# Performance work log

Hardware: AMD Instinct MI355X
Metric: run time of the kernel (lower is better)

Reference implementation:

```python
import jax, jax.numpy as jnp
import numpy as np

B, C, H, W = 64, 256, 14, 14
K = 9
HID = 256   # EdgeAgg hidden_channels = in_channels
OUT = 512   # out_channels = 2*in_channels (required by final reshape)


def _knn(q, kset, k):
    # ViG dense_knn_matrix: squared-distance knn, top-k of -dist (self-loop may be included)
    qs = jnp.sum(q * q, -1)
    ks = jnp.sum(kset * kset, -1)
    dist = qs[:, :, None] - 2.0 * jnp.einsum('bnc,bmc->bnm', q, kset) + ks[:, None, :]
    _, idx = jax.lax.top_k(-dist, k)   # (B,N,k) neighbor indices into kset
    return idx


def _edgeconv_add(feat, nbr, validf, w, b):
    # PyG EdgeConv(nn=Linear, aggr='add') with per-node valid-edge mask:
    #   out[i] = sum_{j in valid nbrs(i)} cat(x_i, x_j - x_i) @ w + b
    # nn is linear, so aggregate neighbor diffs BEFORE the matmul (same math, less traffic).
    Cf = feat.shape[-1]
    wa, wb = w[:Cf], w[Cf:]
    deg = jnp.sum(validf, -1, keepdims=True)                   # (B,N,1)
    xj = feat[jnp.arange(feat.shape[0])[:, None, None], nbr]   # (B,N,k,C) gather
    sum_xj = jnp.einsum('bnkc,bnk->bnc', xj, validf)
    return deg * (feat @ wa + b) + (sum_xj - deg * feat) @ wb


def _forward(x, fc1_w, fc1_b, fc2_w, fc2_b, fce_w, fce_b, inout_w, inout_b,
             attn_w, attn_b, upd_w, upd_b, kp_w, kp_b, enc_w, enc_b,
             mu_w, mu_b, dec_w, dec_b, T):
    k = dec_w.shape[-1]
    b_, c_, h_, w_ = x.shape
    n = h_ * w_
    xs = x.reshape(b_, c_, n)                       # (B,C,N)
    x_sp = jnp.transpose(xs, (0, 2, 1))             # (B,N,C) true spatial node feats for knn
    x_sp_d = jax.lax.stop_gradient(x_sp)            # original detaches before knn
    x_nbr = _knn(x_sp_d, x_sp_d, k)
    # temporal roll across the T frames of each clip
    y_sp = jnp.roll(x_sp.reshape(b_ // T, T, n, c_), -1, axis=1).reshape(b_, n, c_)
    y_nbr = _knn(x_sp_d, jax.lax.stop_gradient(y_sp), k)
    # faithful to original: x.view(B*N, C) reinterprets the contiguous (B,C,N) buffer
    x_feat = xs.reshape(b_, n, c_)
    y_feat = jnp.transpose(y_sp, (0, 2, 1)).reshape(b_, n, c_)
    # VAE-like K predictor (deterministic z = mu); argmax -> per-node degree in [0,k)
    hk = x_feat.reshape(b_ * n, c_) @ kp_w + kp_b
    hk = jax.nn.relu(hk @ enc_w + enc_b)
    mu = hk @ mu_w + mu_b
    logits = mu @ dec_w + dec_b                     # (B*N, k)
    k_int = jnp.argmax(logits, axis=1)
    # generate_mask: keep the first k_int[i] of node i's k edges
    validf = (jnp.arange(k)[None, :] < k_int[:, None]).astype(x.dtype).reshape(b_, n, k)

    def edge_agg(feat, nbr):
        h1 = jax.nn.relu(_edgeconv_add(feat, nbr, validf, fc1_w, fc1_b))
        h2 = _edgeconv_add(h1, nbr, validf, fc2_w, fc2_b)
        return (h2 @ fce_w + fce_b).reshape(b_ * n, -1)

    x_agg = edge_agg(x_feat, x_nbr)
    y_agg = edge_agg(y_feat, y_nbr)
    scores = (jnp.concatenate([x_agg, y_agg], -1) @ attn_w + attn_b)[:, 0]
    wgt = jax.nn.softmax(scores, axis=0)[:, None]   # softmax over ALL B*N nodes (as in source)
    fused = wgt * x_agg + (1.0 - wgt) * y_agg
    xin = x_feat.reshape(b_ * n, c_) @ inout_w + inout_b
    upd = jax.nn.relu(jnp.concatenate([xin, fused], -1) @ upd_w + upd_b)   # (B*N, 2C)
    return jnp.transpose(upd.reshape(b_, n, 2 * c_), (0, 2, 1)).reshape(b_, 2 * c_, h_, w_)


def setup_inputs():
    key = jax.random.key(0)
    ks = iter(jax.random.split(key, 32))

    def lin(i, o):
        return jax.random.normal(next(ks), (i, o), jnp.float32) / np.sqrt(i)

    def bias(o):
        return jax.random.normal(next(ks), (o,), jnp.float32) * 0.01

    return {
        'x': jax.random.normal(next(ks), (B, C, H, W), jnp.float32),
        'fc1_w': lin(2 * C, HID), 'fc1_b': bias(HID),
        'fc2_w': lin(2 * HID, HID), 'fc2_b': bias(HID),
        'fce_w': lin(HID, OUT), 'fce_b': bias(OUT),
        'inout_w': lin(C, OUT), 'inout_b': bias(OUT),
        'attn_w': lin(2 * OUT, 1), 'attn_b': bias(1),
        'upd_w': lin(2 * OUT, OUT), 'upd_b': bias(OUT),
        'kp_w': lin(C, 500), 'kp_b': bias(500),
        'enc_w': lin(500, 64), 'enc_b': bias(64),
        'mu_w': lin(64, 32), 'mu_b': bias(32),
        'dec_w': lin(32, K), 'dec_b': bias(K),
        'T': 16,
    }


def reference(x, fc1_w, fc1_b, fc2_w, fc2_b, fce_w, fce_b, inout_w, inout_b,
              attn_w, attn_b, upd_w, upd_b, kp_w, kp_b, enc_w, enc_b,
              mu_w, mu_b, dec_w, dec_b, T):
    return _forward(x, fc1_w, fc1_b, fc2_w, fc2_b, fce_w, fce_b, inout_w, inout_b,
                    attn_w, attn_b, upd_w, upd_b, kp_w, kp_b, enc_w, enc_b,
                    mu_w, mu_b, dec_w, dec_b, T)
```

## Files before the change

### kernel.cpp

```cpp
#include <hip/hip_runtime.h>
#include <cstddef>
#include <cstdint>

constexpr int BATCH = 64;
constexpr int CH    = 256;
constexpr int NPT   = 196;
constexpr int ROWS  = BATCH * NPT;
constexpr int BSTRIDE = CH * NPT;
constexpr int KNB   = 8;
constexpr int DSTR  = 208;

typedef __bf16 bf16x8 __attribute__((ext_vector_type(8)));
typedef __bf16 bf16x4 __attribute__((ext_vector_type(4)));
typedef _Float16 f16x8 __attribute__((ext_vector_type(8)));
typedef float  f32x4  __attribute__((ext_vector_type(4)));
typedef unsigned long long u64;

__device__ __forceinline__ int src_batch(int b) {
    return (b & ~15) | ((b + 1) & 15);
}

__device__ __forceinline__ void gload_lds16(const void* g, void* l) {
    __builtin_amdgcn_global_load_lds(
        (const __attribute__((address_space(1))) void*)g,
        (__attribute__((address_space(3))) void*)l, 16, 0, 0);
}

__device__ __forceinline__ int xcd_swz(int lin, int nwg) {
    int q = nwg >> 3;
    return (lin & 7) * q + (lin >> 3);
}

__global__ __launch_bounds__(256) void front_kernel(const float* __restrict__ x,
        _Float16* __restrict__ XH, _Float16* __restrict__ XL,
        __bf16* __restrict__ XB, float* __restrict__ qsp,
        const float* __restrict__ fc1_w, const float* __restrict__ fc2_w,
        const float* __restrict__ fce_w, const float* __restrict__ upd_w,
        const float* __restrict__ kp_w, const float* __restrict__ kp_b,
        const float* __restrict__ enc_w, const float* __restrict__ enc_b,
        const float* __restrict__ mu_w, const float* __restrict__ mu_b,
        const float* __restrict__ dec_w, const float* __restrict__ dec_b,
        const float* __restrict__ inout_w, const float* __restrict__ inout_b,
        const float* __restrict__ upd_b,
        __bf16* __restrict__ W1catT, __bf16* __restrict__ W2catT,
        __bf16* __restrict__ fcet, __bf16* __restrict__ updC,
        float* __restrict__ KW1, float* __restrict__ kb1,
        float* __restrict__ KW2, float* __restrict__ kb2,
        float* __restrict__ bcomp, int* __restrict__ smcnt) {
    __shared__ __attribute__((aligned(16))) char smem[16896];
    float (*tile)[65] = (float(*)[65])smem;
    int bid = blockIdx.x;
    int t = threadIdx.x;
    if (bid < 1024) {
        int m0 = (bid & 3) * 64, c0 = ((bid >> 2) & 3) * 64, b = bid >> 4;
        const float* xb = x + (size_t)b * BSTRIDE;
        #pragma unroll
        for (int s = 0; s < 16; ++s) {
            int idx = s * 256 + t;
            int cc = idx >> 6, mm = idx & 63;
            int m = m0 + mm;
            float v = (m < NPT) ? xb[(size_t)(c0 + cc) * NPT + m] : 0.f;
            tile[cc][mm] = v;
            if (m < NPT)
                XB[(size_t)b * BSTRIDE + (size_t)(c0 + cc) * NPT + m] = (__bf16)v;
        }
        __syncthreads();
        #pragma unroll
        for (int s = 0; s < 16; ++s) {
            int idx = s * 256 + t;
            int mm = idx >> 6, cc = idx & 63;
            float v = tile[cc][mm];
            _Float16 h = (_Float16)v;
            size_t off = ((size_t)b * 256 + (m0 + mm)) * 256 + c0 + cc;
            XH[off] = h;
            XL[off] = (_Float16)(v - (float)h);
        }
        if (t < 64) {
            float acc = 0.f;
            #pragma unroll
            for (int cc = 0; cc < 64; ++cc) {
                float v = tile[cc][t];
                acc = fmaf(v, v, acc);
            }
            qsp[(size_t)(c0 >> 6) * 16384 + b * 256 + m0 + t] = acc;
        }
    } else {
        int pbid = bid - 1024;
        if (pbid == 0 && t == 0) smcnt[0] = 0;
        if (pbid < 64) {
            const float* W = (pbid < 32) ? fc1_w : fc2_w;
            __bf16* WT = (pbid < 32) ? W1catT : W2catT;
            int local = pbid & 31;
            int n0 = (local >> 2) * 64, k0 = (local & 3) * 64;
            #pragma unroll
            for (int s = 0; s < 16; ++s) {
                int idx = s * 256 + t;
                int kk = idx >> 6, nn = idx & 63;
                float v;
                if (n0 < 256)
                    v = W[(size_t)(k0 + kk) * 256 + n0 + nn] -
                        W[(size_t)(k0 + kk + 256) * 256 + n0 + nn];
                else
                    v = W[(size_t)(k0 + kk + 256) * 256 + (n0 - 256) + nn];
                tile[kk][nn] = v;
            }
            __syncthreads();
            #pragma unroll
            for (int s = 0; s < 16; ++s) {
                int idx = s * 256 + t;
                int nn = idx >> 6, kk = idx & 63;
                WT[(size_t)(n0 + nn) * 256 + k0 + kk] = (__bf16)tile[kk][nn];
            }
        } else if (pbid < 96) {
            int local = pbid - 64;
            int n0 = (local >> 2) * 64, k0 = (local & 3) * 64;
            #pragma unroll
            for (int s = 0; s < 16; ++s) {
                int idx = s * 256 + t;
                int kk = idx >> 6, nn = idx & 63;
                tile[kk][nn] = fce_w[(size_t)(k0 + kk) * 512 + n0 + nn];
            }
            __syncthreads();
            #pragma unroll
            for (int s = 0; s < 16; ++s) {
                int idx = s * 256 + t;
                int nn = idx >> 6, kk = idx & 63;
                fcet[(size_t)(n0 + nn) * 256 + k0 + kk] = (__bf16)tile[kk][nn];
            }
        } else if (pbid < 160) {
            int local = pbid - 96;
            int k0 = (local >> 3) * 64, n0 = (local & 7) * 64;
            #pragma unroll
            for (int s = 0; s < 16; ++s) {
                int idx = s * 256 + t;
                int kk = idx >> 6, nn = idx & 63;
                tile[kk][nn] = upd_w[(size_t)(512 + k0 + kk) * 512 + n0 + nn];
            }
            __syncthreads();
            #pragma unroll
            for (int s = 0; s < 16; ++s) {
                int idx = s * 256 + t;
                int nn = idx >> 6, kk = idx & 63;
                updC[(size_t)(n0 + nn) * 768 + 256 + k0 + kk] = (__bf16)tile[kk][nn];
            }
        } else if (pbid < 224) {
            int i = (pbid - 160) * 4 + (t >> 6);
            int j = t & 63;
            double acc = 0.0;
            for (int k = 0; k < 500; ++k)
                acc += (double)kp_w[(size_t)i * 500 + k] * (double)enc_w[(size_t)k * 64 + j];
            KW1[i * 64 + j] = (float)acc;
        } else if (pbid == 224) {
            int j = t;
            if (j < 64) {
                double acc = (double)enc_b[j];
                for (int k = 0; k < 500; ++k)
                    acc += (double)kp_b[k] * (double)enc_w[(size_t)k * 64 + j];
                kb1[j] = (float)acc;
            }
        } else if (pbid < 228) {
            int e = (pbid - 225) * 256 + t;
            if (e < 576) {
                int i = e / 9, j = e - (e / 9) * 9;
                double acc = 0.0;
                for (int k = 0; k < 32; ++k)
                    acc += (double)mu_w[(size_t)i * 32 + k] * (double)dec_w[(size_t)k * 9 + j];
                KW2[e] = (float)acc;
            } else if (e < 585) {
                int j = e - 576;
                double acc = (double)dec_b[j];
                for (int k = 0; k < 32; ++k)
                    acc += (double)mu_b[k] * (double)dec_w[(size_t)k * 9 + j];
                kb2[j] = (float)acc;
            }
        } else if (pbid < 740) {
            int e = (pbid - 228) * 256 + t;
            int k = e >> 9, n = e & 511;
            const float* iw = inout_w + (size_t)k * 512;
            float a0 = 0.f, a1 = 0.f, a2 = 0.f, a3 = 0.f;
            for (int j = 0; j < 512; j += 4) {
                a0 = fmaf(iw[j + 0], upd_w[(size_t)(j + 0) * 512 + n], a0);
                a1 = fmaf(iw[j + 1], upd_w[(size_t)(j + 1) * 512 + n], a1);
                a2 = fmaf(iw[j + 2], upd_w[(size_t)(j + 2) * 512 + n], a2);
                a3 = fmaf(iw[j + 3], upd_w[(size_t)(j + 3) * 512 + n], a3);
            }
            updC[(size_t)n * 768 + k] = (__bf16)((a0 + a1) + (a2 + a3));
        } else {
            int n = (pbid - 740) * 256 + t;
            float a0 = upd_b[n], a1 = 0.f, a2 = 0.f, a3 = 0.f;
            for (int j = 0; j < 512; j += 4) {
                a0 = fmaf(inout_b[j + 0], upd_w[(size_t)(j + 0) * 512 + n], a0);
                a1 = fmaf(inout_b[j + 1], upd_w[(size_t)(j + 1) * 512 + n], a1);
                a2 = fmaf(inout_b[j + 2], upd_w[(size_t)(j + 2) * 512 + n], a2);
                a3 = fmaf(inout_b[j + 3], upd_w[(size_t)(j + 3) * 512 + n], a3);
            }
            bcomp[n] = (a0 + a1) + (a2 + a3);
        }
    }
}

__global__ __launch_bounds__(256) void gram_kint(const _Float16* __restrict__ XH,
        const _Float16* __restrict__ XL, const float* __restrict__ qsp,
        float* __restrict__ Dw, const float* __restrict__ x,
        const float* __restrict__ W1, const float* __restrict__ b1,
        const float* __restrict__ W2, const float* __restrict__ b2,
        int* __restrict__ kint, float* __restrict__ degf) {
    __shared__ __attribute__((aligned(16))) char smem[32768];
    int bid = blockIdx.x;
    int t = threadIdx.x;
    if (bid < 2048) {
        int nid = xcd_swz(bid, 2048);
        int job = nid >> 4;
        int tile = nid & 15;
        int by = tile >> 2, bx = tile & 3;
        int r0 = by * 64, c0 = bx * 64;
        int qb = (job < 64) ? job : job - 64;
        int kb = (job < 64) ? qb : src_batch(qb);
        int w = t >> 6, l = t & 63;
        int lr = l & 15, lg = l >> 4;
        int wr = (w >> 1) * 32, wc = (w & 1) * 32;
        const _Float16* qh = XH + (size_t)qb * 65536;
        const _Float16* ql = XL + (size_t)qb * 65536;
        const _Float16* kh = XH + (size_t)kb * 65536;
        const _Float16* kl = XL + (size_t)kb * 65536;
        int srow = w * 16 + (l >> 2);
        int scb = (l & 3) * 8;
        f32x4 acc[2][2] = {};
        auto stage = [&](int k0, int bsel) {
            _Float16* base = (_Float16*)(smem + bsel * 16384);
            size_t goA = (size_t)(r0 + srow) * 256 + k0 + scb;
            size_t goB = (size_t)(c0 + srow) * 256 + k0 + scb;
            gload_lds16(qh + goA, base + w * 512);
            gload_lds16(ql + goA, base + 2048 + w * 512);
            gload_lds16(kh + goB, base + 4096 + w * 512);
            gload_lds16(kl + goB, base + 6144 + w * 512);
        };
        stage(0, 0);
        #pragma unroll
        for (int ks8 = 0; ks8 < 8; ++ks8) {
            if (ks8 < 7) {
                stage((ks8 + 1) * 32, (ks8 + 1) & 1);
                asm volatile("s_waitcnt vmcnt(4)" ::: "memory");
            } else {
                asm volatile("s_waitcnt vmcnt(0)" ::: "memory");
            }
            __syncthreads();
            _Float16* base = (_Float16*)(smem + (ks8 & 1) * 16384);
            _Float16* Ah = base;
            _Float16* Al = base + 2048;
            _Float16* Bh = base + 4096;
            _Float16* Bl = base + 6144;
            f16x8 ah[2], alv[2], bh[2], blv[2];
            #pragma unroll
            for (int mi = 0; mi < 2; ++mi) {
                ah[mi]  = *(const f16x8*)(Ah + (wr + mi * 16 + lr) * 32 + lg * 8);
                alv[mi] = *(const f16x8*)(Al + (wr + mi * 16 + lr) * 32 + lg * 8);
            }
            #pragma unroll
            for (int ni = 0; ni < 2; ++ni) {
                bh[ni]  = *(const f16x8*)(Bh + (wc + ni * 16 + lr) * 32 + lg * 8);
                blv[ni] = *(const f16x8*)(Bl + (wc + ni * 16 + lr) * 32 + lg * 8);
            }
            #pragma unroll
            for (int mi = 0; mi < 2; ++mi)
                #pragma unroll
                for (int ni = 0; ni < 2; ++ni) {
                    acc[mi][ni] = __builtin_amdgcn_mfma_f32_16x16x32_f16(
                        ah[mi], bh[ni], acc[mi][ni], 0, 0, 0);
                    acc[mi][ni] = __builtin_amdgcn_mfma_f32_16x16x32_f16(
                        ah[mi], blv[ni], acc[mi][ni], 0, 0, 0);
                    acc[mi][ni] = __builtin_amdgcn_mfma_f32_16x16x32_f16(
                        alv[mi], bh[ni], acc[mi][ni], 0, 0, 0);
                }
            __syncthreads();
        }
        float ksv[2];
        #pragma unroll
        for (int ni = 0; ni < 2; ++ni) {
            int col = c0 + wc + ni * 16 + lr;
            if (col < NPT) {
                size_t o0 = (size_t)kb * 256 + col;
                ksv[ni] = ((qsp[o0] + qsp[16384 + o0]) + qsp[32768 + o0]) +
                          qsp[49152 + o0];
            } else ksv[ni] = 0.f;
        }
        #pragma unroll
        for (int mi = 0; mi < 2; ++mi) {
            #pragma unroll
            for (int r = 0; r < 4; ++r) {
                if (r0 + wr + mi * 16 + r >= NPT) continue;
                int grow = r0 + wr + mi * 16 + lg * 4 + r;
                if (grow >= NPT) continue;
                size_t o0 = (size_t)qb * 256 + grow;
                float qq = ((qsp[o0] + qsp[16384 + o0]) + qsp[32768 + o0]) +
                           qsp[49152 + o0];
                size_t rbase = ((size_t)job * NPT + grow) * DSTR;
                #pragma unroll
                for (int ni = 0; ni < 2; ++ni) {
                    int col = c0 + wc + ni * 16 + lr;
                    if (col < NPT)
                        Dw[rbase + col] = qq - 2.f * acc[mi][ni][r] + ksv[ni];
                }
            }
        }
    } else {
        float (*xr)[256] = (float(*)[256])smem;
        float (*ebuf)[64] = (float(*)[64])(smem + 16384);
        float (*lg2)[9]  = (float(*)[9])(smem + 20480);
        int r0 = (bid - 2048) * 16;
        const float4* xg = (const float4*)(x + (size_t)r0 * 256);
        float4* xs = (float4*)&xr[0][0];
        #pragma unroll
        for (int s = 0; s < 4; ++s) xs[s * 256 + t] = xg[s * 256 + t];
        __syncthreads();
        int w = t >> 6, l = t & 63;
        {
            float bb = b1[l];
            float a0 = bb, a1 = bb, a2 = bb, a3 = bb;
            const float* x0 = xr[w * 4 + 0];
            const float* x1 = xr[w * 4 + 1];
            const float* x2 = xr[w * 4 + 2];
            const float* x3 = xr[w * 4 + 3];
            for (int c = 0; c < 256; ++c) {
                float wv = W1[c * 64 + l];
                a0 = fmaf(x0[c], wv, a0);
                a1 = fmaf(x1[c], wv, a1);
                a2 = fmaf(x2[c], wv, a2);
                a3 = fmaf(x3[c], wv, a3);
            }
            ebuf[w * 4 + 0][l] = fmaxf(a0, 0.f);
            ebuf[w * 4 + 1][l] = fmaxf(a1, 0.f);
            ebuf[w * 4 + 2][l] = fmaxf(a2, 0.f);
            ebuf[w * 4 + 3][l] = fmaxf(a3, 0.f);
        }
        __syncthreads();
        int rr = t >> 4, cc = t & 15;
        if (cc < 9) {
            float acc = b2[cc];
            for (int j = 0; j < 64; ++j)
                acc = fmaf(ebuf[rr][j], W2[j * 9 + cc], acc);
            lg2[rr][cc] = acc;
        }
        __syncthreads();
        if (cc == 0) {
            float best = lg2[rr][0];
            int bi = 0;
            #pragma unroll
            for (int j = 1; j < 9; ++j)
                if (lg2[rr][j] > best) { best = lg2[rr][j]; bi = j; }
            kint[r0 + rr] = bi;
            degf[r0 + rr] = (float)bi;
        }
    }
}

__global__ __launch_bounds__(256) void topk_p1(const float* __restrict__ Dw,
        int* __restrict__ nbr, const __bf16* __restrict__ XB,
        const __bf16* __restrict__ W1catT, __bf16* __restrict__ P1) {
    __shared__ __attribute__((aligned(16))) char smem[32768];
    int bid = blockIdx.x;
    int t = threadIdx.x;
    if (bid < 392) {
        u64 (*lists)[4][8] = (u64(*)[4][8])smem;
        int lrow = t >> 2, q = t & 3;
        int rowid = bid * 64 + lrow;
        const float* rp = Dw + (size_t)rowid * DSTR + q * 52;
        u64 kreg[8];
        #pragma unroll
        for (int p = 0; p < 8; ++p) kreg[p] = ~0ull;
        for (int s4 = 0; s4 < 13; ++s4) {
            f32x4 dv = *(const f32x4*)(rp + s4 * 4);
            #pragma unroll
            for (int e = 0; e < 4; ++e) {
                int col = q * 52 + s4 * 4 + e;
                unsigned u = __float_as_uint(dv[e]);
                u = (u & 0x80000000u) ? ~u : (u | 0x80000000u);
                u64 key = (col < NPT) ? (((u64)u << 32) | (unsigned)col) : ~0ull;
                if (key < kreg[7]) {
                    #pragma unroll
                    for (int p = 0; p < 8; ++p) {
                        u64 mn = (key < kreg[p]) ? key : kreg[p];
                        u64 mx = (key < kreg[p]) ? kreg[p] : key;
                        kreg[p] = mn; key = mx;
                    }
                }
            }
        }
        #pragma unroll
        for (int p = 0; p < 8; ++p) lists[lrow][q][p] = kreg[p];
        __syncthreads();
        if (q == 0) {
            const u64* c = &lists[lrow][0][0];
            int p0 = 0, p1 = 0, p2 = 0, p3 = 0;
            #pragma unroll
            for (int it = 0; it < 8; ++it) {
                u64 v0 = c[p0], v1 = c[8 + p1], v2 = c[16 + p2], v3 = c[24 + p3];
                u64 best = v0; int bj = 0;
                if (v1 < best) { best = v1; bj = 1; }
                if (v2 < best) { best = v2; bj = 2; }
                if (v3 < best) { best = v3; bj = 3; }
                if (bj == 0) p0 = (p0 < 7) ? p0 + 1 : 7;
                else if (bj == 1) p1 = (p1 < 7) ? p1 + 1 : 7;
                else if (bj == 2) p2 = (p2 < 7) ? p2 + 1 : 7;
                else p3 = (p3 < 7) ? p3 + 1 : 7;
                nbr[(size_t)rowid * KNB + it] = (int)(best & 0xffffffffu);
            }
        }
    } else {
        __bf16* As = (__bf16*)smem;
        __bf16* Bs = As + 128 * 64;
        int lin = bid - 392;
        int nid = xcd_swz(lin, 392);
        int bx = nid & 3, by = nid >> 2;
        int w = t >> 6, l = t & 63;
        int r0 = by * 128, c0 = bx * 128;
        int lr = l & 15, lg = l >> 4;
        int wr = (w >> 1) * 64, wc = (w & 1) * 64;
        constexpr int K = 256, N = 512;
        f32x4 acc[4][4] = {};
        for (int k0 = 0; k0 < K; k0 += 64) {
            #pragma unroll
            for (int i = 0; i < 4; ++i) {
                int row = (w * 4 + i) * 8 + (l >> 3);
                int c8 = l & 7;
                gload_lds16(XB + (size_t)(r0 + row) * K + k0 + c8 * 8,
                            As + (w * 4 + i) * 512);
                gload_lds16(W1catT + (size_t)(c0 + row) * K + k0 + c8 * 8,
                            Bs + (w * 4 + i) * 512);
            }
            asm volatile("s_waitcnt vmcnt(0)" ::: "memory");
            __syncthreads();
            #pragma unroll
            for (int ks = 0; ks < 2; ++ks) {
                bf16x8 af[4], bfr[4];
                #pragma unroll
                for (int mi = 0; mi < 4; ++mi)
                    af[mi] = *(const bf16x8*)(As + (wr + mi * 16 + lr) * 64 + ks * 32 + lg * 8);
                #pragma unroll
                for (int ni = 0; ni < 4; ++ni)
                    bfr[ni] = *(const bf16x8*)(Bs + (wc + ni * 16 + lr) * 64 + ks * 32 + lg * 8);
                #pragma unroll
                for (int mi = 0; mi < 4; ++mi)
                    #pragma unroll
                    for (int ni = 0; ni < 4; ++ni)
                        acc[mi][ni] = __builtin_amdgcn_mfma_f32_16x16x32_bf16(
                            af[mi], bfr[ni], acc[mi][ni], 0, 0, 0);
            }
            __syncthreads();
        }
        #pragma unroll
        for (int mi = 0; mi < 4; ++mi) {
            #pragma unroll
            for (int r = 0; r < 4; ++r) {
                int row = r0 + wr + mi * 16 + lg * 4 + r;
                #pragma unroll
                for (int ni = 0; ni < 4; ++ni) {
                    int col = c0 + wc + ni * 16 + lr;
                    P1[(size_t)row * N + col] = (__bf16)acc[mi][ni][r];
                }
            }
        }
    }
}

template<int STAGE, int RELU>
__global__ __launch_bounds__(256) void combine_kernel(const __bf16* __restrict__ P,
        const int* __restrict__ nbr, const int* __restrict__ kint_,
        const float* __restrict__ degf, const float* __restrict__ bias,
        __bf16* __restrict__ H) {
    int g = threadIdx.x >> 6, lane = threadIdx.x & 63;
    int nid = xcd_swz(blockIdx.x, 2 * ROWS / 4);
    int r = nid * 4 + g;
    int branch = (r >= ROWS);
    int rr = r - branch * ROWS;
    int b = rr / NPT, i = rr - b * NPT;
    size_t srow, mbase;
    if constexpr (STAGE == 1) {
        int fb = branch ? src_batch(b) : b;
        srow = (size_t)fb * NPT + i;
        mbase = (size_t)fb * NPT;
    } else {
        srow = (size_t)r;
        mbase = (size_t)branch * ROWS + (size_t)b * NPT;
    }
    const int* nb = nbr + (size_t)branch * ((size_t)ROWS * KNB) + (size_t)rr * KNB;
    bf16x4 sv = *(const bf16x4*)(P + srow * 512 + lane * 4);
    float4 bv = *(const float4*)(bias + lane * 4);
    float s0 = 0.f, s1 = 0.f, s2 = 0.f, s3 = 0.f;
    int kk = kint_[rr];
    for (int tt = 0; tt < kk; ++tt) {
        int m = nb[tt];
        bf16x4 v = *(const bf16x4*)(P + (mbase + m) * 512 + 256 + lane * 4);
        s0 += (float)v[0]; s1 += (float)v[1]; s2 += (float)v[2]; s3 += (float)v[3];
    }
    float dg = degf[rr];
    float o0 = fmaf(dg, (float)sv[0] + bv.x, s0);
    float o1 = fmaf(dg, (float)sv[1] + bv.y, s1);
    float o2 = fmaf(dg, (float)sv[2] + bv.z, s2);
    float o3 = fmaf(dg, (float)sv[3] + bv.w, s3);
    if constexpr (RELU) {
        o0 = fmaxf(o0, 0.f); o1 = fmaxf(o1, 0.f);
        o2 = fmaxf(o2, 0.f); o3 = fmaxf(o3, 0.f);
    }
    bf16x4 ov;
    ov[0] = (__bf16)o0; ov[1] = (__bf16)o1; ov[2] = (__bf16)o2; ov[3] = (__bf16)o3;
    *(bf16x4*)(H + (size_t)r * 256 + lane * 4) = ov;
}

template<int FLAGS, int CONCAT>
__global__ __launch_bounds__(256) void mfma_gemm(
    const __bf16* __restrict__ A0, const __bf16* __restrict__ A1,
    const __bf16* __restrict__ WT, const float* __restrict__ bias,
    float* __restrict__ Cf, __bf16* __restrict__ Cb, int K, int N,
    const float* __restrict__ aw, float* __restrict__ scp,
    const float* __restrict__ wgt) {
    constexpr int SMEMB = (FLAGS & 8) ? (128 * 129 * 4) : (2 * 128 * 64 * 2);
    __shared__ __attribute__((aligned(16))) char smem[SMEMB];
    __bf16* As = (__bf16*)smem;
    __bf16* Bs = As + 128 * 64;
    int lin = blockIdx.x + 4 * blockIdx.y;
    int nid = xcd_swz(lin, 4 * gridDim.y);
    int bx = nid & 3, by = nid >> 2;
    int t = threadIdx.x, w = t >> 6, l = t & 63;
    int r0 = by * 128, c0 = bx * 128;
    int lr = l & 15, lg = l >> 4;
    int wr = (w >> 1) * 64, wc = (w & 1) * 64;
    f32x4 acc[4][4] = {};
    for (int k0 = 0; k0 < K; k0 += 64) {
        #pragma unroll
        for (int i = 0; i < 4; ++i) {
            int row = (w * 4 + i) * 8 + (l >> 3);
            int c8 = l & 7;
            if constexpr (CONCAT == 2) {
                if (k0 < 256) {
                    gload_lds16(A0 + (size_t)(r0 + row) * 256 + k0 + c8 * 8,
                                As + (w * 4 + i) * 512);
                } else {
                    int kk2 = k0 - 256 + c8 * 8;
                    size_t gr = (size_t)(r0 + row);
                    bf16x8 xa = *(const bf16x8*)(A1 + gr * 512 + kk2);
                    bf16x8 ya = *(const bf16x8*)(A1 + ((size_t)ROWS + gr) * 512 + kk2);
                    float wv = wgt[gr];
                    bf16x8 mx;
                    #pragma unroll
                    for (int j = 0; j < 8; ++j)
                        mx[j] = (__bf16)(wv * (float)xa[j] + (1.f - wv) * (float)ya[j]);
                    *(bf16x8*)(As + (w * 4 + i) * 512 + l * 8) = mx;
                }
            } else {
                gload_lds16(A0 + (size_t)(r0 + row) * K + k0 + c8 * 8,
                            As + (w * 4 + i) * 512);
            }
            gload_lds16(WT + (size_t)(c0 + row) * K + k0 + c8 * 8,
                        Bs + (w * 4 + i) * 512);
        }
        asm volatile("s_waitcnt vmcnt(0)" ::: "memory");
        __syncthreads();
        #pragma unroll
        for (int ks = 0; ks < 2; ++ks) {
            bf16x8 af[4], bfr[4];
            #pragma unroll
            for (int mi = 0; mi < 4; ++mi)
                af[mi] = *(const bf16x8*)(As + (wr + mi * 16 + lr) * 64 + ks * 32 + lg * 8);
            #pragma unroll
            for (int ni = 0; ni < 4; ++ni)
                bfr[ni] = *(const bf16x8*)(Bs + (wc + ni * 16 + lr) * 64 + ks * 32 + lg * 8);
            #pragma unroll
            for (int mi = 0; mi < 4; ++mi)
                #pragma unroll
                for (int ni = 0; ni < 4; ++ni)
                    acc[mi][ni] = __builtin_amdgcn_mfma_f32_16x16x32_bf16(
                        af[mi], bfr[ni], acc[mi][ni], 0, 0, 0);
        }
        __syncthreads();
    }
    if constexpr ((FLAGS & 8) != 0) {
        float* tile = (float*)smem;
        #pragma unroll
        for (int mi = 0; mi < 4; ++mi)
            #pragma unroll
            for (int r = 0; r < 4; ++r) {
                int rrow = wr + mi * 16 + lg * 4 + r;
                #pragma unroll
                for (int ni = 0; ni < 4; ++ni) {
                    int ccol = wc + ni * 16 + lr;
                    float v = acc[mi][ni][r];
                    if (bias) v += bias[c0 + ccol];
                    if constexpr ((FLAGS & 1) != 0) v = fmaxf(v, 0.f);
                    tile[rrow * 129 + ccol] = v;
                }
            }
        __syncthreads();
        int cc = t >> 6, rr2 = t & 63;
        #pragma unroll
        for (int cs = 0; cs < 128; cs += 4) {
            #pragma unroll
            for (int h = 0; h < 2; ++h) {
                int row = r0 + rr2 + h * 64;
                int bb = row / NPT, ii = row - bb * NPT;
                Cf[((size_t)bb * 512 + (c0 + cc + cs)) * NPT + ii] =
                    tile[(rr2 + h * 64) * 129 + cc + cs];
            }
        }
    } else if constexpr ((FLAGS & 16) != 0) {
        int half = (r0 >= ROWS) ? 1 : 0;
        float ps[4][4] = {};
        #pragma unroll
        for (int mi = 0; mi < 4; ++mi)
            #pragma unroll
            for (int r = 0; r < 4; ++r) {
                int row = r0 + wr + mi * 16 + lg * 4 + r;
                #pragma unroll
                for (int ni = 0; ni < 4; ++ni) {
                    int col = c0 + wc + ni * 16 + lr;
                    float v = acc[mi][ni][r] + bias[col];
                    Cb[(size_t)row * N + col] = (__bf16)v;
                    ps[mi][r] = fmaf(v, aw[half * 512 + col], ps[mi][r]);
                }
            }
        #pragma unroll
        for (int m = 1; m <= 8; m <<= 1)
            #pragma unroll
            for (int mi = 0; mi < 4; ++mi)
                #pragma unroll
                for (int r = 0; r < 4; ++r)
                    ps[mi][r] += __shfl_xor(ps[mi][r], m, 64);
        if (lr == 0) {
            int slot = half * 8 + bx * 2 + (w & 1);
            #pragma unroll
            for (int mi = 0; mi < 4; ++mi)
                #pragma unroll
                for (int r = 0; r < 4; ++r) {
                    int sr = r0 - half * ROWS + wr + mi * 16 + lg * 4 + r;
                    scp[(size_t)slot * ROWS + sr] = ps[mi][r];
                }
        }
    } else {
        #pragma unroll
        for (int mi = 0; mi < 4; ++mi) {
            #pragma unroll
            for (int r = 0; r < 4; ++r) {
                int row = r0 + wr + mi * 16 + lg * 4 + r;
                #pragma unroll
                for (int ni = 0; ni < 4; ++ni) {
                    int col = c0 + wc + ni * 16 + lr;
                    float v = acc[mi][ni][r];
                    if (bias) v += bias[col];
                    if constexpr ((FLAGS & 1) != 0) v = fmaxf(v, 0.f);
                    if constexpr ((FLAGS & 4) != 0)
                        Cb[(size_t)row * N + col] = (__bf16)v;
                    else
                        Cf[(size_t)row * N + col] = v;
                }
            }
        }
    }
}

__global__ __launch_bounds__(256) void softmax_all(const float* __restrict__ scp,
        const float* __restrict__ ab, float* __restrict__ scores,
        float* __restrict__ mpart, float* __restrict__ spart,
        int* __restrict__ cnt, float* __restrict__ wgt) {
    __shared__ float red[256];
    __shared__ float MS[2];
    __shared__ bool islast;
    int t = threadIdx.x;
    int sr = blockIdx.x * 256 + t;
    float s = ab[0];
    #pragma unroll
    for (int i = 0; i < 16; ++i) s += scp[(size_t)i * ROWS + sr];
    scores[sr] = s;
    red[t] = s; __syncthreads();
    for (int off = 128; off; off >>= 1) {
        if (t < off) red[t] = fmaxf(red[t], red[t + off]);
        __syncthreads();
    }
    float mb = red[0]; __syncthreads();
    red[t] = expf(s - mb); __syncthreads();
    for (int off = 128; off; off >>= 1) {
        if (t < off) red[t] += red[t + off];
        __syncthreads();
    }
    if (t == 0) {
        mpart[blockIdx.x] = mb;
        spart[blockIdx.x] = red[0];
        __threadfence();
        int old = atomicAdd(cnt, 1);
        islast = (old == 48);
    }
    __syncthreads();
    if (!islast) return;
    __threadfence();
    if (t == 0) {
        float M = mpart[0];
        for (int i = 1; i < 49; ++i) M = fmaxf(M, mpart[i]);
        float S = 0.f;
        for (int i = 0; i < 49; ++i) S += spart[i] * expf(mpart[i] - M);
        MS[0] = M; MS[1] = S;
        cnt[0] = 0;
    }
    __syncthreads();
    float M = MS[0], denom = MS[1];
    for (int i = t; i < ROWS; i += 256)
        wgt[i] = expf(scores[i] - M) / denom;
}

extern "C" void kernel_launch(void* const* d_in, const int* in_sizes, int n_in,
                              void* d_out, int out_size, void* d_ws, size_t ws_size,
                              hipStream_t stream) {
    (void)in_sizes; (void)n_in; (void)out_size; (void)ws_size;
    const float* x       = (const float*)d_in[0];
    const float* fc1_w   = (const float*)d_in[1];
    const float* fc1_b   = (const float*)d_in[2];
    const float* fc2_w   = (const float*)d_in[3];
    const float* fc2_b   = (const float*)d_in[4];
    const float* fce_w   = (const float*)d_in[5];
    const float* fce_b   = (const float*)d_in[6];
    const float* inout_w = (const float*)d_in[7];
    const float* inout_b = (const float*)d_in[8];
    const float* attn_w  = (const float*)d_in[9];
    const float* attn_b  = (const float*)d_in[10];
    const float* upd_w   = (const float*)d_in[11];
    const float* upd_b   = (const float*)d_in[12];
    const float* kp_w    = (const float*)d_in[13];
    const float* kp_b    = (const float*)d_in[14];
    const float* enc_w   = (const float*)d_in[15];
    const float* enc_b   = (const float*)d_in[16];
    const float* mu_w    = (const float*)d_in[17];
    const float* mu_b    = (const float*)d_in[18];
    const float* dec_w   = (const float*)d_in[19];
    const float* dec_b   = (const float*)d_in[20];
    float* out = (float*)d_out;

    char* base = (char*)d_ws;
    size_t o = 0;
    auto alloc = [&](size_t bytes) -> void* {
        void* p = base + o;
        o += (bytes + 255) & ~(size_t)255;
        return p;
    };
    float* qsp    = (float*)alloc((size_t)4 * 64 * 256 * 4);
    float* degf   = (float*)alloc(ROWS * 4);
    float* scores = (float*)alloc(ROWS * 4);
    float* wgt    = (float*)alloc(ROWS * 4);
    int*   kint   = (int*)  alloc(ROWS * 4);
    float* KW1    = (float*)alloc(256 * 64 * 4);
    float* kb1    = (float*)alloc(64 * 4);
    float* KW2    = (float*)alloc(64 * 9 * 4);
    float* kb2    = (float*)alloc(9 * 4);
    float* bcomp  = (float*)alloc(512 * 4);
    float* scp    = (float*)alloc((size_t)16 * ROWS * 4);
    float* mpart  = (float*)alloc(64 * 4);
    float* spart  = (float*)alloc(64 * 4);
    int*   smcnt  = (int*)  alloc(256);
    int*   nbr    = (int*)  alloc((size_t)128 * NPT * KNB * 4);
    char*  regD   = (char*) alloc((size_t)ROWS * 512 * 2);
    __bf16* XB    = (__bf16*)alloc((size_t)ROWS * 256 * 2);
    __bf16* H1    = (__bf16*)alloc((size_t)2 * ROWS * 256 * 2);
    __bf16* H2    = (__bf16*)alloc((size_t)2 * ROWS * 256 * 2);
    char*  regAGG = (char*) alloc((size_t)2 * ROWS * 512 * 4);
    __bf16* W1catT= (__bf16*)alloc((size_t)512 * 256 * 2);
    __bf16* W2catT= (__bf16*)alloc((size_t)512 * 256 * 2);
    __bf16* fcet  = (__bf16*)alloc((size_t)512 * 256 * 2);
    __bf16* updC  = (__bf16*)alloc((size_t)512 * 768 * 2);
    __bf16* P1buf = (__bf16*)regD;
    _Float16* XSPH = (_Float16*)regAGG;
    _Float16* XSPL = XSPH + (size_t)64 * 256 * 256;
    float* Dw     = (float*)(regAGG + (size_t)17 * 1024 * 1024);
    __bf16* P2buf = (__bf16*)regAGG;
    __bf16* AGGb  = (__bf16*)regAGG;
    __bf16* XAGGb = AGGb;

    front_kernel<<<1766, 256, 0, stream>>>(x, XSPH, XSPL, XB, qsp,
                                           fc1_w, fc2_w, fce_w, upd_w,
                                           kp_w, kp_b, enc_w, enc_b,
                                           mu_w, mu_b, dec_w, dec_b,
                                           inout_w, inout_b, upd_b,
                                           W1catT, W2catT, fcet, updC,
                                           KW1, kb1, KW2, kb2, bcomp, smcnt);

    gram_kint<<<2832, 256, 0, stream>>>(XSPH, XSPL, qsp, Dw, x,
                                        KW1, kb1, KW2, kb2, kint, degf);

    topk_p1<<<784, 256, 0, stream>>>(Dw, nbr, XB, W1catT, P1buf);

    combine_kernel<1, 1><<<2 * ROWS / 4, 256, 0, stream>>>(
        P1buf, nbr, kint, degf, fc1_b, H1);

    mfma_gemm<4, 0><<<dim3(4, 196), 256, 0, stream>>>(
        H1, nullptr, W2catT, nullptr, nullptr, P2buf, 256, 512,
        nullptr, nullptr, nullptr);
    combine_kernel<2, 0><<<2 * ROWS / 4, 256, 0, stream>>>(
        P2buf, nbr, kint, degf, fc2_b, H2);

    mfma_gemm<20, 0><<<dim3(4, 196), 256, 0, stream>>>(
        H2, nullptr, fcet, fce_b, nullptr, AGGb, 256, 512,
        attn_w, scp, nullptr);

    softmax_all<<<49, 256, 0, stream>>>(scp, attn_b, scores, mpart, spart,
                                        smcnt, wgt);

    mfma_gemm<9, 2><<<dim3(4, 98), 256, 0, stream>>>(
        XB, XAGGb, updC, bcomp, out, nullptr, 768, 512,
        nullptr, nullptr, wgt);
}
```

Before: 211.2 us.

## Give each wave a full 64x64 gram tile loaded straight from global memory

```diff
diff --git a/kernel.cpp b/kernel.cpp
--- a/kernel.cpp
+++ b/kernel.cpp
@@ -205,66 +205,44 @@
         const float* __restrict__ W1, const float* __restrict__ b1,
         const float* __restrict__ W2, const float* __restrict__ b2,
         int* __restrict__ kint, float* __restrict__ degf) {
-    __shared__ __attribute__((aligned(16))) char smem[32768];
+    __shared__ __attribute__((aligned(16))) char smem[21056];
     int bid = blockIdx.x;
     int t = threadIdx.x;
-    if (bid < 2048) {
-        int nid = xcd_swz(bid, 2048);
+    if (bid < 512) {
+        int w = t >> 6, l = t & 63;
+        int wid = bid * 4 + w;
+        int nid = xcd_swz(wid, 2048);
         int job = nid >> 4;
         int tile = nid & 15;
         int by = tile >> 2, bx = tile & 3;
         int r0 = by * 64, c0 = bx * 64;
         int qb = (job < 64) ? job : job - 64;
         int kb = (job < 64) ? qb : src_batch(qb);
-        int w = t >> 6, l = t & 63;
         int lr = l & 15, lg = l >> 4;
-        int wr = (w >> 1) * 32, wc = (w & 1) * 32;
         const _Float16* qh = XH + (size_t)qb * 65536;
         const _Float16* ql = XL + (size_t)qb * 65536;
         const _Float16* kh = XH + (size_t)kb * 65536;
         const _Float16* kl = XL + (size_t)kb * 65536;
-        int srow = w * 16 + (l >> 2);
-        int scb = (l & 3) * 8;
-        f32x4 acc[2][2] = {};
-        auto stage = [&](int k0, int bsel) {
-            _Float16* base = (_Float16*)(smem + bsel * 16384);
-            size_t goA = (size_t)(r0 + srow) * 256 + k0 + scb;
-            size_t goB = (size_t)(c0 + srow) * 256 + k0 + scb;
-            gload_lds16(qh + goA, base + w * 512);
-            gload_lds16(ql + goA, base + 2048 + w * 512);
-            gload_lds16(kh + goB, base + 4096 + w * 512);
-            gload_lds16(kl + goB, base + 6144 + w * 512);
-        };
-        stage(0, 0);
-        #pragma unroll
-        for (int ks8 = 0; ks8 < 8; ++ks8) {
-            if (ks8 < 7) {
-                stage((ks8 + 1) * 32, (ks8 + 1) & 1);
-                asm volatile("s_waitcnt vmcnt(4)" ::: "memory");
-            } else {
-                asm volatile("s_waitcnt vmcnt(0)" ::: "memory");
-            }
-            __syncthreads();
-            _Float16* base = (_Float16*)(smem + (ks8 & 1) * 16384);
-            _Float16* Ah = base;
-            _Float16* Al = base + 2048;
-            _Float16* Bh = base + 4096;
-            _Float16* Bl = base + 6144;
-            f16x8 ah[2], alv[2], bh[2], blv[2];
-            #pragma unroll
-            for (int mi = 0; mi < 2; ++mi) {
-                ah[mi]  = *(const f16x8*)(Ah + (wr + mi * 16 + lr) * 32 + lg * 8);
-                alv[mi] = *(const f16x8*)(Al + (wr + mi * 16 + lr) * 32 + lg * 8);
-            }
-            #pragma unroll
-            for (int ni = 0; ni < 2; ++ni) {
-                bh[ni]  = *(const f16x8*)(Bh + (wc + ni * 16 + lr) * 32 + lg * 8);
-                blv[ni] = *(const f16x8*)(Bl + (wc + ni * 16 + lr) * 32 + lg * 8);
-            }
-            #pragma unroll
-            for (int mi = 0; mi < 2; ++mi)
-                #pragma unroll
-                for (int ni = 0; ni < 2; ++ni) {
+        f32x4 acc[4][4] = {};
+        #pragma unroll 1
+        for (int k0 = 0; k0 < 256; k0 += 32) {
+            f16x8 ah[4], alv[4], bh[4], blv[4];
+            #pragma unroll
+            for (int mi = 0; mi < 4; ++mi) {
+                size_t off = (size_t)(r0 + mi * 16 + lr) * 256 + k0 + lg * 8;
+                ah[mi]  = *(const f16x8*)(qh + off);
+                alv[mi] = *(const f16x8*)(ql + off);
+            }
+            #pragma unroll
+            for (int ni = 0; ni < 4; ++ni) {
+                size_t off = (size_t)(c0 + ni * 16 + lr) * 256 + k0 + lg * 8;
+                bh[ni]  = *(const f16x8*)(kh + off);
+                blv[ni] = *(const f16x8*)(kl + off);
+            }
+            #pragma unroll
+            for (int mi = 0; mi < 4; ++mi)
+                #pragma unroll
+                for (int ni = 0; ni < 4; ++ni) {
                     acc[mi][ni] = __builtin_amdgcn_mfma_f32_16x16x32_f16(
                         ah[mi], bh[ni], acc[mi][ni], 0, 0, 0);
                     acc[mi][ni] = __builtin_amdgcn_mfma_f32_16x16x32_f16(
@@ -272,12 +250,11 @@
                     acc[mi][ni] = __builtin_amdgcn_mfma_f32_16x16x32_f16(
                         alv[mi], bh[ni], acc[mi][ni], 0, 0, 0);
                 }
-            __syncthreads();
-        }
-        float ksv[2];
-        #pragma unroll
-        for (int ni = 0; ni < 2; ++ni) {
-            int col = c0 + wc + ni * 16 + lr;
+        }
+        float ksv[4];
+        #pragma unroll
+        for (int ni = 0; ni < 4; ++ni) {
+            int col = c0 + ni * 16 + lr;
             if (col < NPT) {
                 size_t o0 = (size_t)kb * 256 + col;
                 ksv[ni] = ((qsp[o0] + qsp[16384 + o0]) + qsp[32768 + o0]) +
@@ -285,19 +262,19 @@
             } else ksv[ni] = 0.f;
         }
         #pragma unroll
-        for (int mi = 0; mi < 2; ++mi) {
+        for (int mi = 0; mi < 4; ++mi) {
             #pragma unroll
             for (int r = 0; r < 4; ++r) {
-                if (r0 + wr + mi * 16 + r >= NPT) continue;
-                int grow = r0 + wr + mi * 16 + lg * 4 + r;
+                if (r0 + mi * 16 + r >= NPT) continue;
+                int grow = r0 + mi * 16 + lg * 4 + r;
                 if (grow >= NPT) continue;
                 size_t o0 = (size_t)qb * 256 + grow;
                 float qq = ((qsp[o0] + qsp[16384 + o0]) + qsp[32768 + o0]) +
                            qsp[49152 + o0];
                 size_t rbase = ((size_t)job * NPT + grow) * DSTR;
                 #pragma unroll
-                for (int ni = 0; ni < 2; ++ni) {
-                    int col = c0 + wc + ni * 16 + lr;
+                for (int ni = 0; ni < 4; ++ni) {
+                    int col = c0 + ni * 16 + lr;
                     if (col < NPT)
                         Dw[rbase + col] = qq - 2.f * acc[mi][ni][r] + ksv[ni];
                 }
@@ -307,7 +284,7 @@
         float (*xr)[256] = (float(*)[256])smem;
         float (*ebuf)[64] = (float(*)[64])(smem + 16384);
         float (*lg2)[9]  = (float(*)[9])(smem + 20480);
-        int r0 = (bid - 2048) * 16;
+        int r0 = (bid - 512) * 16;
         const float4* xg = (const float4*)(x + (size_t)r0 * 256);
         float4* xs = (float4*)&xr[0][0];
         #pragma unroll
@@ -779,7 +756,7 @@
                                            W1catT, W2catT, fcet, updC,
                                            KW1, kb1, KW2, kb2, bcomp, smcnt);
 
-    gram_kint<<<2832, 256, 0, stream>>>(XSPH, XSPL, qsp, Dw, x,
+    gram_kint<<<1296, 256, 0, stream>>>(XSPH, XSPL, qsp, Dw, x,
                                         KW1, kb1, KW2, kb2, kint, degf);
 
     topk_p1<<<784, 256, 0, stream>>>(Dw, nbr, XB, W1catT, P1buf);
```

After: 235.5 us. +11.5%, slower.
